# Performance work log

Hardware: AMD Instinct MI355X
Metric: run time of the kernel (lower is better)

Reference implementation:

```python
import jax, jax.numpy as jnp
import numpy as np

STRIDE = 8
PAD = 8
KSZ = 16


def setup_inputs() -> dict:
    key = jax.random.key(0)
    k1, k2, k3 = jax.random.split(key, 3)
    B, Cin, Cout, L = 16, 512, 1, 4000
    inp = jax.random.normal(k1, (B, Cin, L), dtype=jnp.float32)
    # t60 in [0.1, 0.5) so that round(t60*100)-10 lands in [0, 40]
    t60s = 0.1 + 0.39 * jax.random.uniform(k2, (B // 2,), dtype=jnp.float32)
    kernel_weight = jax.random.uniform(k3, (41, Cin, Cout, KSZ), dtype=jnp.float32)
    return {"input": inp, "t60s": t60s, "kernel_weight": kernel_weight}


def reference(input, t60s, kernel_weight):
    # per-sample kernel index: round(t60*100).int().repeat(2) - 10
    idx = jnp.tile(jnp.round(t60s * 100.0).astype(jnp.int32), 2) - 10  # (B,)
    w = kernel_weight[idx]                      # (B, Cin, Cout, K) gathered per sample
    # torch conv_transpose1d(x, W) == conv(x with lhs_dilation=stride,
    #                                      flip_k(W).swap(Cin,Cout), pad=K-1-p)
    w = jnp.flip(jnp.swapaxes(w, 1, 2), axis=-1)  # (B, Cout, Cin, K)
    pad = KSZ - 1 - PAD

    def per_sample(x, wk):  # x: (Cin, L), wk: (Cout, Cin, K)
        y = jax.lax.conv_general_dilated(
            x[None], wk,
            window_strides=(1,),
            padding=[(pad, pad)],
            lhs_dilation=(STRIDE,),
            dimension_numbers=("NCH", "OIH", "NCH"),
        )
        return y[0]  # (Cout, L_out), L_out = (L-1)*stride - 2*PAD + K

    return jax.vmap(per_sample)(input, w)  # (B, Cout, L_out)
```

## Files before the change

kernel.cpp:

```cpp
#include <hip/hip_runtime.h>

#define L_IN     4000
#define CIN      512
#define KSZ      16
#define LOUT     31992
#define NQ       3999
#define CCH      32
#define LOUT_PAD 32768
#define NCH      16
#define WS_FLOATS ((size_t)NCH * 16 * LOUT_PAD)

__global__ __launch_bounds__(1024, 4)
void dereverb_stream(const float* __restrict__ x,
                     const float* __restrict__ t60s,
                     const float* __restrict__ kw,
                     float* __restrict__ ws)
{
    __shared__ float wlds[CCH * KSZ];

    const int c0   = blockIdx.x * CCH;
    const int b    = blockIdx.y;
    const int tid  = threadIdx.x;
    const int lane = tid & 63;
    const int wave = tid >> 6;

    float t60 = t60s[b & 7];
    int kidx = (int)rintf(t60 * 100.0f) - 10;
    kidx = __builtin_amdgcn_readfirstlane(kidx);

    if (tid < 128)
        ((float4*)wlds)[tid] =
            ((const float4*)(kw + ((size_t)kidx * CIN + c0) * KSZ))[tid];
    __syncthreads();

    const int qb  = wave * 256 + 4 * lane;
    const int qbl = qb < 3996 ? qb : 3996;
    const int qan = (qb + 4) < NQ ? (qb + 4) : NQ;

    const float* xrow = x + ((size_t)b * CIN + c0) * L_IN;
    const float* xp = xrow + qbl;
    const float* xq = xrow + qan;
    const float4* wl = (const float4*)wlds;

    float acc[4][8];
    #pragma unroll
    for (int qi = 0; qi < 4; ++qi)
        #pragma unroll
        for (int r = 0; r < 8; ++r) acc[qi][r] = 0.0f;

#define FMA_BODY(A, AN, W0, W1, W2, W3) do {                        \
        const float xl[4] = {(A).x, (A).y, (A).z, (A).w};           \
        const float xh[4] = {(A).y, (A).z, (A).w, (AN)};            \
        const float wa[8] = {(W0).x,(W0).y,(W0).z,(W0).w,           \
                             (W1).x,(W1).y,(W1).z,(W1).w};          \
        const float wb[8] = {(W2).x,(W2).y,(W2).z,(W2).w,           \
                             (W3).x,(W3).y,(W3).z,(W3).w};          \
        _Pragma("unroll")                                           \
        for (int qi = 0; qi < 4; ++qi)                              \
            _Pragma("unroll")                                       \
            for (int r = 0; r < 8; ++r) {                           \
                acc[qi][r] = fmaf(xh[qi], wa[r], acc[qi][r]);       \
                acc[qi][r] = fmaf(xl[qi], wb[r], acc[qi][r]);       \
            }                                                       \
    } while (0)

    float4 a0 = *(const float4*)xp;
    float  n0 = *xq;
    float4 a1 = *(const float4*)(xp + L_IN);
    float  n1 = *(xq + L_IN);
    float4 w0 = wl[0], w1 = wl[1], w2 = wl[2], w3 = wl[3];

    #pragma unroll 2
    for (int ci = 0; ci < 30; ++ci) {
        float4 a2 = *(const float4*)(xp + 2 * L_IN);
        float  n2 = *(xq + 2 * L_IN);
        float4 u0 = wl[4], u1 = wl[5], u2 = wl[6], u3 = wl[7];
        FMA_BODY(a0, n0, w0, w1, w2, w3);
        a0 = a1; n0 = n1; a1 = a2; n1 = n2;
        w0 = u0; w1 = u1; w2 = u2; w3 = u3;
        xp += L_IN; xq += L_IN; wl += 4;
    }
    {
        float4 u0 = wl[4], u1 = wl[5], u2 = wl[6], u3 = wl[7];
        FMA_BODY(a0, n0, w0, w1, w2, w3);
        a0 = a1; n0 = n1;
        w0 = u0; w1 = u1; w2 = u2; w3 = u3;
    }
    FMA_BODY(a0, n0, w0, w1, w2, w3);

    float* op = ws + (size_t)(blockIdx.x * 16 + b) * LOUT_PAD + (size_t)8 * qb;
    #pragma unroll
    for (int qi = 0; qi < 4; ++qi) {
        float4 lo = {acc[qi][0], acc[qi][1], acc[qi][2], acc[qi][3]};
        float4 hi = {acc[qi][4], acc[qi][5], acc[qi][6], acc[qi][7]};
        ((float4*)(op + 8 * qi))[0] = lo;
        ((float4*)(op + 8 * qi))[1] = hi;
    }
#undef FMA_BODY
}

__global__ __launch_bounds__(256, 8)
void dereverb_reduce(const float* __restrict__ ws, float* __restrict__ out)
{
    const int b  = blockIdx.y;
    const int t4 = blockIdx.x * 256 + threadIdx.x;
    if (t4 >= LOUT / 4) return;

    const float4* p = (const float4*)(ws + (size_t)b * LOUT_PAD) + t4;
    float4 s = {0.0f, 0.0f, 0.0f, 0.0f};
    #pragma unroll
    for (int c = 0; c < NCH; ++c) {
        float4 v = *p;
        s.x += v.x; s.y += v.y; s.z += v.z; s.w += v.w;
        p += (size_t)16 * LOUT_PAD / 4;
    }
    ((float4*)(out + (size_t)b * LOUT))[t4] = s;
}

#define QPB 256
#define RST 1088
__global__ __launch_bounds__(1024, 4)
void dereverb_fallback(const float* __restrict__ x,
                       const float* __restrict__ t60s,
                       const float* __restrict__ kw,
                       float* __restrict__ out)
{
    __shared__ float lds[8 * RST];

    const int b    = blockIdx.y;
    const int q0   = blockIdx.x * QPB;
    const int tid  = threadIdx.x;
    const int lane = tid & 63;
    const int wave = tid >> 6;

    float t60 = t60s[b & 7];
    int kidx = (int)rintf(t60 * 100.0f) - 10;
    kidx = __builtin_amdgcn_readfirstlane(kidx);
    const float4* wsrc = (const float4*)(kw + (size_t)kidx * (CIN * KSZ));

    ((float4*)lds)[tid]        = wsrc[tid];
    ((float4*)lds)[tid + 1024] = wsrc[tid + 1024];
    __syncthreads();

    const int qb  = q0 + 4 * lane;
    const int qbl = qb < 3996 ? qb : 3996;
    const int qan = (qb + 4) < NQ ? (qb + 4) : NQ;

    const float* xr = x + ((size_t)b * CIN + wave * 32) * L_IN;
    const float* xp = xr + qbl;
    const float* xq = xr + qan;
    const float4* wl = (const float4*)(lds + wave * 32 * KSZ);

    float acc[4][8];
    #pragma unroll
    for (int qi = 0; qi < 4; ++qi)
        #pragma unroll
        for (int r = 0; r < 8; ++r) acc[qi][r] = 0.0f;

    #pragma unroll 4
    for (int ci = 0; ci < 32; ++ci) {
        float4 a  = *(const float4*)xp;
        float  an = *xq;
        xp += L_IN;
        xq += L_IN;

        float4 wv[4];
        wv[0] = wl[0]; wv[1] = wl[1]; wv[2] = wl[2]; wv[3] = wl[3];
        wl += 4;
        const float* wf = (const float*)wv;

        const float x0v[4] = {a.x, a.y, a.z, a.w};
        const float x1v[4] = {a.y, a.z, a.w, an};
        #pragma unroll
        for (int qi = 0; qi < 4; ++qi)
            #pragma unroll
            for (int r = 0; r < 8; ++r) {
                acc[qi][r] = fmaf(x1v[qi], wf[r],     acc[qi][r]);
                acc[qi][r] = fmaf(x0v[qi], wf[r + 8], acc[qi][r]);
            }
    }

    #pragma unroll
    for (int qi = 0; qi < 4; ++qi)
        if (qb + qi > NQ - 1)
            #pragma unroll
            for (int r = 0; r < 8; ++r) acc[qi][r] = 0.0f;

    const size_t obase = (size_t)b * LOUT + (size_t)q0 * 8;
    #pragma unroll
    for (int p = 0; p < 2; ++p) {
        __syncthreads();
        if (wave >= 8) {
            float* rp = lds + (wave - 8) * RST + lane * 17;
            #pragma unroll
            for (int qih = 0; qih < 2; ++qih)
                #pragma unroll
                for (int r = 0; r < 8; ++r)
                    rp[qih * 8 + r] = acc[2 * p + qih][r];
        }
        __syncthreads();
        if (wave < 8) {
            float* rp = lds + wave * RST + lane * 17;
            #pragma unroll
            for (int qih = 0; qih < 2; ++qih)
                #pragma unroll
                for (int r = 0; r < 8; ++r)
                    rp[qih * 8 + r] += acc[2 * p + qih][r];
        }
        __syncthreads();
        int k = tid >> 4, j = tid & 15;
        int tl = 32 * k + 16 * p + j;
        if (q0 * 8 + tl < LOUT) {
            float s = 0.0f;
            #pragma unroll
            for (int w = 0; w < 8; ++w)
                s += lds[w * RST + k * 17 + j];
            out[obase + tl] = s;
        }
    }
}

extern "C" void kernel_launch(void* const* d_in, const int* in_sizes, int n_in,
                              void* d_out, int out_size, void* d_ws, size_t ws_size,
                              hipStream_t stream) {
    const float* x    = (const float*)d_in[0];
    const float* t60s = (const float*)d_in[1];
    const float* kw   = (const float*)d_in[2];
    float* out = (float*)d_out;

    if (ws_size >= WS_FLOATS * sizeof(float) && d_ws != nullptr) {
        float* ws = (float*)d_ws;
        dim3 g1(CIN / CCH, 16);
        dereverb_stream<<<g1, 1024, 0, stream>>>(x, t60s, kw, ws);
        dim3 g2((LOUT / 4 + 255) / 256, 16);
        dereverb_reduce<<<g2, 256, 0, stream>>>(ws, out);
    } else {
        dim3 grid((NQ + QPB - 1) / QPB, 16);
        dereverb_fallback<<<grid, 1024, 0, stream>>>(x, t60s, kw, out);
    }
}
```

Measured before the change: 204.8 us.

## Stage input rows through double-buffered LDS with coalesced register prefetch

The stream kernel now copies the 32 input channel rows into a double-buffered shared-memory tile, four rows per stage. While it computes on the current stage, it prefetches the next stage's rows into registers using fully coalesced float4 loads, then writes them to LDS behind a barrier. Previously each thread did strided per-row global loads with a register rotation. The change aims to improve load coalescing and hide global latency. In exchange it uses about 128KB of LDS per block, which limits occupancy to one block per CU, and adds a barrier at every stage.

```diff
diff --git a/kernel.cpp b/kernel.cpp
--- a/kernel.cpp
+++ b/kernel.cpp
@@ -6,23 +6,24 @@
 #define LOUT     31992
 #define NQ       3999
 #define CCH      32
+#define NST      8
+#define RPS      4
 #define LOUT_PAD 32768
 #define NCH      16
 #define WS_FLOATS ((size_t)NCH * 16 * LOUT_PAD)
 
 __global__ __launch_bounds__(1024, 4)
-void dereverb_stream(const float* __restrict__ x,
-                     const float* __restrict__ t60s,
-                     const float* __restrict__ kw,
-                     float* __restrict__ ws)
+void dereverb_stage(const float* __restrict__ x,
+                    const float* __restrict__ t60s,
+                    const float* __restrict__ kw,
+                    float* __restrict__ ws)
 {
+    __shared__ float xbuf[2 * RPS * L_IN];
     __shared__ float wlds[CCH * KSZ];
 
-    const int c0   = blockIdx.x * CCH;
-    const int b    = blockIdx.y;
-    const int tid  = threadIdx.x;
-    const int lane = tid & 63;
-    const int wave = tid >> 6;
+    const int cx  = blockIdx.x;
+    const int b   = blockIdx.y;
+    const int tid = threadIdx.x;
 
     float t60 = t60s[b & 7];
     int kidx = (int)rintf(t60 * 100.0f) - 10;
@@ -30,17 +31,26 @@
 
     if (tid < 128)
         ((float4*)wlds)[tid] =
-            ((const float4*)(kw + ((size_t)kidx * CIN + c0) * KSZ))[tid];
+            ((const float4*)(kw + ((size_t)kidx * CIN + cx * CCH) * KSZ))[tid];
+
+    const float4* src = (const float4*)(x + ((size_t)b * CIN + cx * CCH) * L_IN);
+
+    {
+        float4 p0 = src[tid];
+        float4 p1 = src[tid + 1024];
+        float4 p2 = src[tid + 2048];
+        float4 p3 = {};
+        if (tid < 928) p3 = src[tid + 3072];
+        ((float4*)xbuf)[tid]        = p0;
+        ((float4*)xbuf)[tid + 1024] = p1;
+        ((float4*)xbuf)[tid + 2048] = p2;
+        if (tid < 928) ((float4*)xbuf)[tid + 3072] = p3;
+    }
     __syncthreads();
 
-    const int qb  = wave * 256 + 4 * lane;
+    const int qb  = 4 * tid;
     const int qbl = qb < 3996 ? qb : 3996;
-    const int qan = (qb + 4) < NQ ? (qb + 4) : NQ;
-
-    const float* xrow = x + ((size_t)b * CIN + c0) * L_IN;
-    const float* xp = xrow + qbl;
-    const float* xq = xrow + qan;
-    const float4* wl = (const float4*)wlds;
+    const int qhl = (qb + 4) < NQ ? (qb + 4) : NQ;
 
     float acc[4][8];
     #pragma unroll
@@ -64,31 +74,39 @@
             }                                                       \
     } while (0)
 
-    float4 a0 = *(const float4*)xp;
-    float  n0 = *xq;
-    float4 a1 = *(const float4*)(xp + L_IN);
-    float  n1 = *(xq + L_IN);
-    float4 w0 = wl[0], w1 = wl[1], w2 = wl[2], w3 = wl[3];
-
     #pragma unroll 2
-    for (int ci = 0; ci < 30; ++ci) {
-        float4 a2 = *(const float4*)(xp + 2 * L_IN);
-        float  n2 = *(xq + 2 * L_IN);
-        float4 u0 = wl[4], u1 = wl[5], u2 = wl[6], u3 = wl[7];
-        FMA_BODY(a0, n0, w0, w1, w2, w3);
-        a0 = a1; n0 = n1; a1 = a2; n1 = n2;
-        w0 = u0; w1 = u1; w2 = u2; w3 = u3;
-        xp += L_IN; xq += L_IN; wl += 4;
-    }
-    {
-        float4 u0 = wl[4], u1 = wl[5], u2 = wl[6], u3 = wl[7];
-        FMA_BODY(a0, n0, w0, w1, w2, w3);
-        a0 = a1; n0 = n1;
-        w0 = u0; w1 = u1; w2 = u2; w3 = u3;
-    }
-    FMA_BODY(a0, n0, w0, w1, w2, w3);
-
-    float* op = ws + (size_t)(blockIdx.x * 16 + b) * LOUT_PAD + (size_t)8 * qb;
+    for (int s = 0; s < NST; ++s) {
+        float4 p0, p1, p2, p3 = {};
+        if (s < NST - 1) {
+            const float4* sp = src + (size_t)(s + 1) * (RPS * L_IN / 4);
+            p0 = sp[tid];
+            p1 = sp[tid + 1024];
+            p2 = sp[tid + 2048];
+            if (tid < 928) p3 = sp[tid + 3072];
+        }
+
+        const float* bufc = xbuf + (s & 1) * (RPS * L_IN);
+        #pragma unroll
+        for (int r = 0; r < RPS; ++r) {
+            const float* row = bufc + r * L_IN;
+            float4 a = *(const float4*)(row + qbl);
+            float  h = row[qhl];
+            const float4* wr = (const float4*)(wlds + (s * RPS + r) * KSZ);
+            float4 w0 = wr[0], w1 = wr[1], w2 = wr[2], w3 = wr[3];
+            FMA_BODY(a, h, w0, w1, w2, w3);
+        }
+
+        if (s < NST - 1) {
+            float* bufn = xbuf + ((s + 1) & 1) * (RPS * L_IN);
+            ((float4*)bufn)[tid]        = p0;
+            ((float4*)bufn)[tid + 1024] = p1;
+            ((float4*)bufn)[tid + 2048] = p2;
+            if (tid < 928) ((float4*)bufn)[tid + 3072] = p3;
+        }
+        __syncthreads();
+    }
+
+    float* op = ws + (size_t)(cx * 16 + b) * LOUT_PAD + (size_t)8 * qb;
     #pragma unroll
     for (int qi = 0; qi < 4; ++qi) {
         float4 lo = {acc[qi][0], acc[qi][1], acc[qi][2], acc[qi][3]};
@@ -230,8 +248,8 @@
 
     if (ws_size >= WS_FLOATS * sizeof(float) && d_ws != nullptr) {
         float* ws = (float*)d_ws;
-        dim3 g1(CIN / CCH, 16);
-        dereverb_stream<<<g1, 1024, 0, stream>>>(x, t60s, kw, ws);
+        dim3 g1(NCH, 16);
+        dereverb_stage<<<g1, 1024, 0, stream>>>(x, t60s, kw, ws);
         dim3 g2((LOUT / 4 + 255) / 256, 16);
         dereverb_reduce<<<g2, 256, 0, stream>>>(ws, out);
     } else {
```

Result: slower. 353.8 us (+72.8%).
